# Performance work log

Measured on AMD Instinct MI355X. Metric: run time of the kernel, lower is better.

Reference implementation:

```python
import jax, jax.numpy as jnp
import numpy as np
import math

D_K = 64

def setup_inputs() -> dict:
    key = jax.random.key(0)
    k1, k2, k3, k4 = jax.random.split(key, 4)
    d = 1024
    x = jax.random.normal(k1, (4, 2048, d), dtype=jnp.float32)
    s = 1.0 / math.sqrt(d)
    Wq = jax.random.normal(k2, (d, D_K), dtype=jnp.float32) * s
    Wk = jax.random.normal(k3, (d, D_K), dtype=jnp.float32) * s
    Wv = jax.random.normal(k4, (d, D_K), dtype=jnp.float32) * s
    return {"x": x, "Wq": Wq, "Wk": Wk, "Wv": Wv}

def reference(x, Wq, Wk, Wv):
    # Q,K,V: [b, s, d_k]
    Q = jnp.einsum('bsd,dk->bsk', x, Wq)
    K = jnp.einsum('bsd,dk->bsk', x, Wk)
    V = jnp.einsum('bsd,dk->bsk', x, Wv)
    scale = 1.0 / math.sqrt(D_K)
    scores = jnp.einsum('bqk,bpk->bqp', Q, K) * scale  # [b, s, s]
    attn = jax.nn.softmax(scores, axis=-1)
    context = jnp.einsum('bqp,bpk->bqk', attn, V)      # [b, s, d_k]
    return context
```

## Files before the change

kernel.cpp:

```cpp
#include <hip/hip_runtime.h>
#include <hip/hip_bf16.h>


typedef __attribute__((ext_vector_type(8))) short bf16x8;
typedef __attribute__((ext_vector_type(4))) float f32x4;
typedef __attribute__((ext_vector_type(4))) unsigned short u16x4;

#define QSCALE 0.1803368801111832f

__device__ __forceinline__ short f2bf(float f) {
    union { float f; unsigned u; } v; v.f = f;
    unsigned r = v.u + 0x7FFF + ((v.u >> 16) & 1);
    return (short)(r >> 16);
}

__device__ __forceinline__ unsigned pk2(float a, float b) {
    union { __hip_bfloat162 h; unsigned u; } v;
    v.h = __float22bfloat162_rn(make_float2(a, b));
    return v.u;
}

__device__ __forceinline__ void gload16(const void* src, void* dst) {
    __builtin_amdgcn_global_load_lds(
        (const __attribute__((address_space(1))) unsigned int*)src,
        (__attribute__((address_space(3))) unsigned int*)dst, 16, 0, 0);
}

__global__ __launch_bounds__(256) void wtrans(const float* __restrict__ Wq,
                                              const float* __restrict__ Wk,
                                              const float* __restrict__ Wv,
                                              short* __restrict__ Wt) {
    __shared__ short lds[64][66];
    int warr = blockIdx.x / 16;
    int d0 = (blockIdx.x % 16) * 64;
    const float* W = (warr == 0) ? Wq : (warr == 1) ? Wk : Wv;
    int rg = threadIdx.x >> 6;
    int c  = threadIdx.x & 63;
    #pragma unroll
    for (int p = 0; p < 16; ++p) {
        int d = p * 4 + rg;
        lds[d][c] = f2bf(W[(d0 + d) * 64 + c]);
    }
    __syncthreads();
    #pragma unroll
    for (int p = 0; p < 16; ++p) {
        int n = p * 4 + rg;
        Wt[(warr * 64 + n) * 1024 + d0 + c] = lds[c][n];
    }
}

__global__ __launch_bounds__(256, 3) void qkv_proj(const float* __restrict__ x,
                                                   const short* __restrict__ Wt,
                                                   short* __restrict__ Q,
                                                   short* __restrict__ K,
                                                   short* __restrict__ Vt) {
    __shared__ char stage_lds[3][16384];

    int tid = threadIdx.x;
    int wid = tid >> 6, lane = tid & 63;
    int l15 = lane & 15, lg = lane >> 4;
    int wr = wid >> 1, wn = wid & 1;
    int logical = (blockIdx.x & 7) * 64 + (blockIdx.x >> 3);
    int mbase = (logical >> 1) * 32;
    int nbase = (logical & 1) * 96;

    int arow_s = tid >> 3, aslot = tid & 7;
    const float* a_src = x + (mbase + arow_s) * 1024 + aslot * 8;
    int a_woff = arow_s * 128 + ((aslot ^ (arow_s & 7)) << 4);

    int b_soff[3];
    #pragma unroll
    for (int j = 0; j < 3; ++j) {
        int cb = wid + j * 4;
        int row = cb * 8 + (lane >> 3);
        int ss = (lane & 7) ^ (row & 7);
        b_soff[j] = (nbase + row) * 1024 + ss * 8;
    }

    f32x4 acc[3];
    #pragma unroll
    for (int f = 0; f < 3; ++f) acc[f] = (f32x4){0.f, 0.f, 0.f, 0.f};

    float4 areg[2][2];

#define ISSUE(g)                                                              \
    {                                                                         \
        const float* ap_ = a_src + (g) * 64;                                  \
        areg[(g) & 1][0] = *(const float4*)ap_;                               \
        areg[(g) & 1][1] = *(const float4*)(ap_ + 4);                         \
        char* bb_ = &stage_lds[(g) % 3][4096];                                \
        _Pragma("unroll")                                                     \
        for (int j = 0; j < 3; ++j)                                           \
            gload16(Wt + b_soff[j] + (g) * 64, bb_ + (wid + j * 4) * 1024);   \
    }

#define WRITEA(g)                                                             \
    {                                                                         \
        float4 f0_ = areg[(g) & 1][0], f1_ = areg[(g) & 1][1];                \
        union { bf16x8 v; unsigned u[4]; } au_;                               \
        au_.u[0] = pk2(f0_.x, f0_.y); au_.u[1] = pk2(f0_.z, f0_.w);           \
        au_.u[2] = pk2(f1_.x, f1_.y); au_.u[3] = pk2(f1_.z, f1_.w);           \
        *(bf16x8*)(&stage_lds[(g) % 3][0] + a_woff) = au_.v;                  \
    }

    ISSUE(0);
    ISSUE(1);
    WRITEA(0);
    asm volatile("s_waitcnt vmcnt(5) lgkmcnt(0)" ::: "memory");
    __builtin_amdgcn_s_barrier();
    __builtin_amdgcn_sched_barrier(0);

    #pragma unroll
    for (int t = 0; t < 16; ++t) {
        if (t + 2 < 16) ISSUE(t + 2);
        if (t + 1 < 16) WRITEA(t + 1);
        const char* Ab = &stage_lds[t % 3][0];
        const char* Bb = &stage_lds[t % 3][4096];
        int arow = wr * 16 + l15;
        __builtin_amdgcn_s_setprio(1);
        #pragma unroll
        for (int h = 0; h < 2; ++h) {
            int sA = (h * 4 + lg) ^ (arow & 7);
            bf16x8 a = *(const bf16x8*)(Ab + arow * 128 + sA * 16);
            #pragma unroll
            for (int f = 0; f < 3; ++f) {
                int brow = (wn * 3 + f) * 16 + l15;
                int ss = (h * 4 + lg) ^ (brow & 7);
                bf16x8 b = *(const bf16x8*)(Bb + brow * 128 + ss * 16);
                acc[f] = __builtin_amdgcn_mfma_f32_16x16x32_bf16(a, b, acc[f], 0, 0, 0);
            }
        }
        __builtin_amdgcn_s_setprio(0);
        if (t < 15) {
            if (t + 2 < 16) {
                asm volatile("s_waitcnt vmcnt(5) lgkmcnt(0)" ::: "memory");
            } else {
                asm volatile("s_waitcnt vmcnt(0) lgkmcnt(0)" ::: "memory");
            }
            __builtin_amdgcn_s_barrier();
            __builtin_amdgcn_sched_barrier(0);
        }
    }
#undef ISSUE
#undef WRITEA

    __syncthreads();
    short* Vl = (short*)&stage_lds[0][0];
    #pragma unroll
    for (int f = 0; f < 3; ++f) {
        int n = nbase + (wn * 3 + f) * 16 + l15;
        #pragma unroll
        for (int r = 0; r < 4; ++r) {
            int ml = wr * 16 + lg * 4 + r;
            int m = mbase + ml;
            float v = acc[f][r];
            if (n < 64) {
                Q[m * 64 + n] = f2bf(v * QSCALE);
            } else if (n < 128) {
                K[m * 64 + (n - 64)] = f2bf(v);
            } else {
                Vl[ml * 72 + (n - 128)] = f2bf(v);
            }
        }
    }
    if (nbase == 96) {
        __syncthreads();
        int dk = tid >> 2;
        int m0 = (tid & 3) * 8;
        int b_ = mbase >> 11;
        int s_ = mbase & 2047;
        #pragma unroll
        for (int j = 0; j < 2; ++j) {
            u16x4 v;
            #pragma unroll
            for (int i = 0; i < 4; ++i) v[i] = (unsigned short)Vl[(m0 + j * 4 + i) * 72 + dk];
            *(u16x4*)&Vt[(b_ * 64 + dk) * 2048 + s_ + m0 + j * 4] = v;
        }
    }
}

__global__ __launch_bounds__(512) void attn32(const short* __restrict__ Q,
                                              const short* __restrict__ K,
                                              const short* __restrict__ Vt,
                                              float* __restrict__ out) {
    __shared__ char ubuf[8][8704];
    __shared__ float Mw[8][32];
    __shared__ float Lw[8][32];
    __shared__ float Ltot[32];

    int tid = threadIdx.x, wid = tid >> 6, lane = tid & 63;
    int l15 = lane & 15, lg = lane >> 4;
    int logical = (blockIdx.x & 7) * 32 + (blockIdx.x >> 3);
    int b_ = logical >> 6;
    int q0 = (logical & 63) * 32;
    const short* Kb = K + b_ * 2048 * 64;
    const short* Vb = Vt + b_ * 64 * 2048;

    bf16x8 bq[2][2];
    #pragma unroll
    for (int qg = 0; qg < 2; ++qg) {
        const short* Qp = Q + (b_ * 2048 + q0 + qg * 16 + l15) * 64 + lg * 8;
        bq[qg][0] = *(const bf16x8*)Qp;
        bq[qg][1] = *(const bf16x8*)(Qp + 32);
    }

    short* P = (short*)&ubuf[wid][0];

    f32x4 acc[2][4];
    #pragma unroll
    for (int qg = 0; qg < 2; ++qg)
        #pragma unroll
        for (int t = 0; t < 4; ++t) acc[qg][t] = (f32x4){0.f, 0.f, 0.f, 0.f};
    float m_run[2] = {-INFINITY, -INFINITY};
    float l_run[2] = {0.f, 0.f};

    int kv0 = wid * 256;
    for (int kv = kv0; kv < kv0 + 256; kv += 64) {
        f32x4 s[2][4];
        __builtin_amdgcn_s_setprio(1);
        #pragma unroll
        for (int kt = 0; kt < 4; ++kt) {
            const short* Kp = Kb + (kv + kt * 16 + l15) * 64 + lg * 8;
            bf16x8 ak0 = *(const bf16x8*)Kp;
            bf16x8 ak1 = *(const bf16x8*)(Kp + 32);
            f32x4 z0 = (f32x4){0.f, 0.f, 0.f, 0.f};
            z0 = __builtin_amdgcn_mfma_f32_16x16x32_bf16(ak0, bq[0][0], z0, 0, 0, 0);
            s[0][kt] = __builtin_amdgcn_mfma_f32_16x16x32_bf16(ak1, bq[0][1], z0, 0, 0, 0);
            f32x4 z1 = (f32x4){0.f, 0.f, 0.f, 0.f};
            z1 = __builtin_amdgcn_mfma_f32_16x16x32_bf16(ak0, bq[1][0], z1, 0, 0, 0);
            s[1][kt] = __builtin_amdgcn_mfma_f32_16x16x32_bf16(ak1, bq[1][1], z1, 0, 0, 0);
        }
        __builtin_amdgcn_s_setprio(0);

        #pragma unroll
        for (int qg = 0; qg < 2; ++qg) {
            float m01 = fmaxf(fmaxf(s[qg][0][0], s[qg][0][1]), fmaxf(s[qg][0][2], s[qg][0][3]));
            float m23 = fmaxf(fmaxf(s[qg][1][0], s[qg][1][1]), fmaxf(s[qg][1][2], s[qg][1][3]));
            float m45 = fmaxf(fmaxf(s[qg][2][0], s[qg][2][1]), fmaxf(s[qg][2][2], s[qg][2][3]));
            float m67 = fmaxf(fmaxf(s[qg][3][0], s[qg][3][1]), fmaxf(s[qg][3][2], s[qg][3][3]));
            float mt = fmaxf(fmaxf(m01, m23), fmaxf(m45, m67));
            mt = fmaxf(mt, __shfl_xor(mt, 16));
            mt = fmaxf(mt, __shfl_xor(mt, 32));
            if (!__all(mt - m_run[qg] <= 8.0f)) {
                float mn = fmaxf(m_run[qg], mt);
                float c = exp2f(m_run[qg] - mn);
                m_run[qg] = mn;
                l_run[qg] *= c;
                #pragma unroll
                for (int t = 0; t < 4; ++t)
                    #pragma unroll
                    for (int r = 0; r < 4; ++r) acc[qg][t][r] *= c;
            }
            float rs = 0.f;
            #pragma unroll
            for (int kt = 0; kt < 4; ++kt)
                #pragma unroll
                for (int r = 0; r < 4; ++r) {
                    float p = exp2f(s[qg][kt][r] - m_run[qg]);
                    s[qg][kt][r] = p;
                    rs += p;
                }
            rs += __shfl_xor(rs, 16);
            rs += __shfl_xor(rs, 32);
            l_run[qg] += rs;
        }

        #pragma unroll
        for (int qg = 0; qg < 2; ++qg)
            #pragma unroll
            for (int kt = 0; kt < 4; ++kt) {
                union { u16x4 v; unsigned u[2]; } h;
                h.u[0] = pk2(s[qg][kt][0], s[qg][kt][1]);
                h.u[1] = pk2(s[qg][kt][2], s[qg][kt][3]);
                *(u16x4*)&P[(qg * 16 + l15) * 72 + kt * 16 + lg * 4] = h.v;
            }

        __builtin_amdgcn_s_setprio(1);
        #pragma unroll
        for (int ps = 0; ps < 2; ++ps) {
            bf16x8 bp0 = *(const bf16x8*)&P[l15 * 72 + ps * 32 + lg * 8];
            bf16x8 bp1 = *(const bf16x8*)&P[(16 + l15) * 72 + ps * 32 + lg * 8];
            #pragma unroll
            for (int t = 0; t < 4; ++t) {
                const short* Vp = Vb + (t * 16 + l15) * 2048 + kv + ps * 32 + lg * 8;
                bf16x8 av = *(const bf16x8*)Vp;
                acc[0][t] = __builtin_amdgcn_mfma_f32_16x16x32_bf16(av, bp0, acc[0][t], 0, 0, 0);
                acc[1][t] = __builtin_amdgcn_mfma_f32_16x16x32_bf16(av, bp1, acc[1][t], 0, 0, 0);
            }
        }
        __builtin_amdgcn_s_setprio(0);
    }

    if (lg == 0) {
        #pragma unroll
        for (int qg = 0; qg < 2; ++qg) {
            Mw[wid][qg * 16 + l15] = m_run[qg];
            Lw[wid][qg * 16 + l15] = l_run[qg];
        }
    }
    __syncthreads();

    float* accw = (float*)&ubuf[wid][0];
    #pragma unroll
    for (int qg = 0; qg < 2; ++qg) {
        int row = qg * 16 + l15;
        float m = Mw[0][row];
        #pragma unroll
        for (int w = 1; w < 8; ++w) m = fmaxf(m, Mw[w][row]);
        float fac = exp2f(m_run[qg] - m);
        #pragma unroll
        for (int t = 0; t < 4; ++t) {
            f32x4 v = acc[qg][t];
            v[0] *= fac; v[1] *= fac; v[2] *= fac; v[3] *= fac;
            *(f32x4*)&accw[row * 68 + t * 16 + lg * 4] = v;
        }
    }

    if (wid == 0 && lg == 0) {
        #pragma unroll
        for (int qg = 0; qg < 2; ++qg) {
            int row = qg * 16 + l15;
            float m = Mw[0][row];
            #pragma unroll
            for (int w = 1; w < 8; ++w) m = fmaxf(m, Mw[w][row]);
            float L = 0.f;
            #pragma unroll
            for (int w = 0; w < 8; ++w)
                L += Lw[w][row] * exp2f(Mw[w][row] - m);
            Ltot[row] = L;
        }
    }
    __syncthreads();

    #pragma unroll
    for (int j = 0; j < 4; ++j) {
        int o = tid + j * 512;
        int row = o >> 6, col = o & 63;
        float ssum = 0.f;
        #pragma unroll
        for (int w = 0; w < 8; ++w)
            ssum += ((const float*)&ubuf[w][0])[row * 68 + col];
        out[(b_ * 2048 + q0 + row) * 64 + col] = ssum / Ltot[row];
    }
}

extern "C" void kernel_launch(void* const* d_in, const int* in_sizes, int n_in,
                              void* d_out, int out_size, void* d_ws, size_t ws_size,
                              hipStream_t stream) {
    const float* x  = (const float*)d_in[0];
    const float* Wq = (const float*)d_in[1];
    const float* Wk = (const float*)d_in[2];
    const float* Wv = (const float*)d_in[3];
    float* out = (float*)d_out;

    char* ws = (char*)d_ws;
    short* Wt = (short*)ws;
    short* Q  = (short*)(ws + 393216);
    short* K  = (short*)(ws + 393216 + 1048576);
    short* Vt = (short*)(ws + 393216 + 2 * 1048576);

    hipLaunchKernelGGL(wtrans,   dim3(48),  dim3(256), 0, stream, Wq, Wk, Wv, Wt);
    hipLaunchKernelGGL(qkv_proj, dim3(512), dim3(256), 0, stream, x, Wt, Q, K, Vt);
    hipLaunchKernelGGL(attn32,   dim3(256), dim3(512), 0, stream, Q, K, Vt, out);
}
```

Baseline: 42.69 us.

## Prefetch K tiles into double-buffered registers and hoist V loads early

The attention loop is fully unrolled. K fragments for the next 64-key tile are prefetched into a double-buffered register array while softmax runs, and V fragments for the current tile are loaded at the top of each iteration so the loads overlap the QK and softmax work. Launch bounds now request two blocks per CU. This should hide global-load latency, but it raises register pressure, and the occupancy hint may force register spills.

```diff
diff --git a/kernel.cpp b/kernel.cpp
--- a/kernel.cpp
+++ b/kernel.cpp
@@ -179,10 +179,10 @@
     }
 }
 
-__global__ __launch_bounds__(512) void attn32(const short* __restrict__ Q,
-                                              const short* __restrict__ K,
-                                              const short* __restrict__ Vt,
-                                              float* __restrict__ out) {
+__global__ __launch_bounds__(512, 2) void attn32(const short* __restrict__ Q,
+                                                 const short* __restrict__ K,
+                                                 const short* __restrict__ Vt,
+                                                 float* __restrict__ out) {
     __shared__ char ubuf[8][8704];
     __shared__ float Mw[8][32];
     __shared__ float Lw[8][32];
@@ -215,22 +215,47 @@
     float l_run[2] = {0.f, 0.f};
 
     int kv0 = wid * 256;
-    for (int kv = kv0; kv < kv0 + 256; kv += 64) {
+
+    bf16x8 kr[2][8];
+    #pragma unroll
+    for (int kt = 0; kt < 4; ++kt) {
+        const short* Kp = Kb + (kv0 + kt * 16 + l15) * 64 + lg * 8;
+        kr[0][kt * 2]     = *(const bf16x8*)Kp;
+        kr[0][kt * 2 + 1] = *(const bf16x8*)(Kp + 32);
+    }
+
+    #pragma unroll
+    for (int t = 0; t < 4; ++t) {
+        int kv = kv0 + t * 64;
+
+        bf16x8 vr[8];
+        #pragma unroll
+        for (int ps = 0; ps < 2; ++ps)
+            #pragma unroll
+            for (int tt = 0; tt < 4; ++tt)
+                vr[ps * 4 + tt] = *(const bf16x8*)(Vb + (tt * 16 + l15) * 2048 + kv + ps * 32 + lg * 8);
+
         f32x4 s[2][4];
         __builtin_amdgcn_s_setprio(1);
         #pragma unroll
         for (int kt = 0; kt < 4; ++kt) {
-            const short* Kp = Kb + (kv + kt * 16 + l15) * 64 + lg * 8;
-            bf16x8 ak0 = *(const bf16x8*)Kp;
-            bf16x8 ak1 = *(const bf16x8*)(Kp + 32);
             f32x4 z0 = (f32x4){0.f, 0.f, 0.f, 0.f};
-            z0 = __builtin_amdgcn_mfma_f32_16x16x32_bf16(ak0, bq[0][0], z0, 0, 0, 0);
-            s[0][kt] = __builtin_amdgcn_mfma_f32_16x16x32_bf16(ak1, bq[0][1], z0, 0, 0, 0);
+            z0 = __builtin_amdgcn_mfma_f32_16x16x32_bf16(kr[t & 1][kt * 2], bq[0][0], z0, 0, 0, 0);
+            s[0][kt] = __builtin_amdgcn_mfma_f32_16x16x32_bf16(kr[t & 1][kt * 2 + 1], bq[0][1], z0, 0, 0, 0);
             f32x4 z1 = (f32x4){0.f, 0.f, 0.f, 0.f};
-            z1 = __builtin_amdgcn_mfma_f32_16x16x32_bf16(ak0, bq[1][0], z1, 0, 0, 0);
-            s[1][kt] = __builtin_amdgcn_mfma_f32_16x16x32_bf16(ak1, bq[1][1], z1, 0, 0, 0);
+            z1 = __builtin_amdgcn_mfma_f32_16x16x32_bf16(kr[t & 1][kt * 2], bq[1][0], z1, 0, 0, 0);
+            s[1][kt] = __builtin_amdgcn_mfma_f32_16x16x32_bf16(kr[t & 1][kt * 2 + 1], bq[1][1], z1, 0, 0, 0);
         }
         __builtin_amdgcn_s_setprio(0);
+
+        if (t < 3) {
+            #pragma unroll
+            for (int kt = 0; kt < 4; ++kt) {
+                const short* Kp = Kb + (kv + 64 + kt * 16 + l15) * 64 + lg * 8;
+                kr[(t + 1) & 1][kt * 2]     = *(const bf16x8*)Kp;
+                kr[(t + 1) & 1][kt * 2 + 1] = *(const bf16x8*)(Kp + 32);
+            }
+        }
 
         #pragma unroll
         for (int qg = 0; qg < 2; ++qg) {
@@ -247,9 +272,9 @@
                 m_run[qg] = mn;
                 l_run[qg] *= c;
                 #pragma unroll
-                for (int t = 0; t < 4; ++t)
+                for (int tt = 0; tt < 4; ++tt)
                     #pragma unroll
-                    for (int r = 0; r < 4; ++r) acc[qg][t][r] *= c;
+                    for (int r = 0; r < 4; ++r) acc[qg][tt][r] *= c;
             }
             float rs = 0.f;
             #pragma unroll
@@ -281,11 +306,9 @@
             bf16x8 bp0 = *(const bf16x8*)&P[l15 * 72 + ps * 32 + lg * 8];
             bf16x8 bp1 = *(const bf16x8*)&P[(16 + l15) * 72 + ps * 32 + lg * 8];
             #pragma unroll
-            for (int t = 0; t < 4; ++t) {
-                const short* Vp = Vb + (t * 16 + l15) * 2048 + kv + ps * 32 + lg * 8;
-                bf16x8 av = *(const bf16x8*)Vp;
-                acc[0][t] = __builtin_amdgcn_mfma_f32_16x16x32_bf16(av, bp0, acc[0][t], 0, 0, 0);
-                acc[1][t] = __builtin_amdgcn_mfma_f32_16x16x32_bf16(av, bp1, acc[1][t], 0, 0, 0);
+            for (int tt = 0; tt < 4; ++tt) {
+                acc[0][tt] = __builtin_amdgcn_mfma_f32_16x16x32_bf16(vr[ps * 4 + tt], bp0, acc[0][tt], 0, 0, 0);
+                acc[1][tt] = __builtin_amdgcn_mfma_f32_16x16x32_bf16(vr[ps * 4 + tt], bp1, acc[1][tt], 0, 0, 0);
             }
         }
         __builtin_amdgcn_s_setprio(0);
```

After: 41.78 us, median of 3. 2.1% less time.
